# Optimization experiments

Hardware: AMD Instinct MI355X
Metric: run time of the kernel (lower is better)

The kernel has to match this reference:

```python
import jax, jax.numpy as jnp
import numpy as np

N = 50000        # nodes
E = 800000       # random edges (self loops appended inside reference, per PyG default)
IN = 128         # in_channels
H1, C1 = 8, 64   # conv1: heads, hidden_channels
NUM_CLASSES = 2  # conv2 out (heads=1, concat=False)
NEG_SLOPE = 0.2  # PyG GATConv default LeakyReLU slope


def setup_inputs() -> dict:
    key = jax.random.key(0)
    ks = jax.random.split(key, 12)
    x = jax.random.normal(ks[0], (N, IN), dtype=jnp.float32)
    edge_index = jax.random.randint(ks[1], (2, E), 0, N)
    # conv1 params: W1 [IN, H1*C1], att vectors [H1, C1], bias [H1*C1]
    W1 = jax.random.normal(ks[2], (IN, H1 * C1), dtype=jnp.float32) / np.sqrt(IN)
    a_src1 = jax.random.normal(ks[3], (H1, C1), dtype=jnp.float32) / np.sqrt(C1)
    a_dst1 = jax.random.normal(ks[4], (H1, C1), dtype=jnp.float32) / np.sqrt(C1)
    b1 = jnp.zeros((H1 * C1,), dtype=jnp.float32)
    # conv2 params: heads=1, out=NUM_CLASSES
    W2 = jax.random.normal(ks[5], (H1 * C1, 1 * NUM_CLASSES), dtype=jnp.float32) / np.sqrt(H1 * C1)
    a_src2 = jax.random.normal(ks[6], (1, NUM_CLASSES), dtype=jnp.float32) / np.sqrt(NUM_CLASSES)
    a_dst2 = jax.random.normal(ks[7], (1, NUM_CLASSES), dtype=jnp.float32) / np.sqrt(NUM_CLASSES)
    b2 = jnp.zeros((NUM_CLASSES,), dtype=jnp.float32)
    return {"x": x, "edge_index": edge_index, "W1": W1, "a_src1": a_src1,
            "a_dst1": a_dst1, "b1": b1, "W2": W2, "a_src2": a_src2,
            "a_dst2": a_dst2, "b2": b2}


def gat_layer(x, src, dst, W, a_src, a_dst, bias, concat):
    n = x.shape[0]
    heads, ch = a_src.shape
    h = (x @ W).reshape(n, heads, ch)                      # [N,H,C]
    alpha_s = jnp.einsum('nhc,hc->nh', h, a_src)           # per-node src score
    alpha_d = jnp.einsum('nhc,hc->nh', h, a_dst)           # per-node dst score
    e = jax.nn.leaky_relu(alpha_s[src] + alpha_d[dst], NEG_SLOPE)  # [Etot,H]
    # segment softmax over edges grouped by destination node
    m = jax.ops.segment_max(e, dst, num_segments=n)
    ex = jnp.exp(e - m[dst])
    den = jax.ops.segment_sum(ex, dst, num_segments=n)
    alpha = ex / den[dst]                                  # [Etot,H]
    out = jax.ops.segment_sum(h[src] * alpha[:, :, None], dst, num_segments=n)  # [N,H,C]
    out = out.reshape(n, heads * ch) if concat else out.mean(axis=1)
    return out + bias


def reference(x, edge_index, W1, a_src1, a_dst1, b1, W2, a_src2, a_dst2, b2):
    n = x.shape[0]
    loops = jnp.arange(n, dtype=edge_index.dtype)
    src = jnp.concatenate([edge_index[0], loops])   # PyG add_self_loops=True
    dst = jnp.concatenate([edge_index[1], loops])
    h = gat_layer(x, src, dst, W1, a_src1, a_dst1, b1, concat=True)   # [N, H1*C1]
    h = jax.nn.elu(h)
    # dropout is identity in eval mode
    out = gat_layer(h, src, dst, W2, a_src2, a_dst2, b2, concat=False)  # [N, 2]
    return out
```

## Files before the change

kernel.cpp:

```cpp
#include <hip/hip_runtime.h>
#include <hip/hip_bf16.h>

#define NEG 0.2f
#define BKT 64
#define DSTR 32

typedef __attribute__((ext_vector_type(8))) short bf16x8;
typedef __attribute__((ext_vector_type(4))) float f32x4;

static __device__ __forceinline__ unsigned short f2bf(float f) {
    union { float f; unsigned u; } v; v.f = f;
    unsigned r = v.u + 0x7fff + ((v.u >> 16) & 1);
    return (unsigned short)(r >> 16);
}
static __device__ __forceinline__ float bf_lo(unsigned u) {
    return __uint_as_float(u << 16);
}
static __device__ __forceinline__ float bf_hi(unsigned u) {
    return __uint_as_float(u & 0xffff0000u);
}

__global__ void k_init(int* __restrict__ deg, unsigned short* __restrict__ csr, int n) {
    int v = blockIdx.x * 256 + threadIdx.x;
    if (v >= n) return;
    deg[(size_t)v * DSTR] = 1;
    csr[(size_t)v * BKT] = (unsigned short)v;
}

__global__ __launch_bounds__(256) void k_big(const int* __restrict__ ei,
                                             int* __restrict__ deg,
                                             unsigned short* __restrict__ csr,
                                             const float* __restrict__ x,
                                             const float* __restrict__ W1,
                                             const float* __restrict__ a_src,
                                             const float* __restrict__ a_dst,
                                             unsigned short* __restrict__ h1b,
                                             float* __restrict__ as1,
                                             float* __restrict__ ad1,
                                             int E_, int n, int gblocks) {
    int tid = threadIdx.x;
    if ((int)blockIdx.x >= gblocks) {
        int e = (blockIdx.x - gblocks) * 256 + tid;
        if (e >= E_) return;
        int s = ei[e], d = ei[E_ + e];
        int slot = atomicAdd(&deg[(size_t)d * DSTR], 1);
        if (slot < BKT) csr[(size_t)d * BKT + slot] = (unsigned short)s;
        return;
    }
    __shared__ unsigned short stg[4][16][72];
    int wave = tid >> 6, lane = tid & 63;
    int l15 = lane & 15, q = lane >> 4;
    int rowblk = blockIdx.x * 256 + wave * 64;

    bf16x8 xf[4][4];
    #pragma unroll
    for (int st = 0; st < 4; st++) {
        int ar = rowblk + st * 16 + l15; if (ar > n - 1) ar = n - 1;
        const float* ap = x + (size_t)ar * 128 + q * 8;
        #pragma unroll
        for (int kb = 0; kb < 4; kb++) {
            float4 v0 = *(const float4*)(ap + kb * 32);
            float4 v1 = *(const float4*)(ap + kb * 32 + 4);
            xf[st][kb][0] = (short)f2bf(v0.x); xf[st][kb][1] = (short)f2bf(v0.y);
            xf[st][kb][2] = (short)f2bf(v0.z); xf[st][kb][3] = (short)f2bf(v0.w);
            xf[st][kb][4] = (short)f2bf(v1.x); xf[st][kb][5] = (short)f2bf(v1.y);
            xf[st][kb][6] = (short)f2bf(v1.z); xf[st][kb][7] = (short)f2bf(v1.w);
        }
    }

    for (int j = 0; j < 8; j++) {
        int col0 = j * 64;
        bf16x8 bfr[4][4];
        #pragma unroll
        for (int kb = 0; kb < 4; kb++)
            #pragma unroll
            for (int t = 0; t < 4; t++) {
                const float* wp = W1 + (size_t)(kb * 32 + q * 8) * 512 + col0 + t * 16 + l15;
                #pragma unroll
                for (int e = 0; e < 8; e++)
                    bfr[kb][t][e] = (short)f2bf(wp[(size_t)e * 512]);
            }
        float asv[4], adv[4];
        #pragma unroll
        for (int t = 0; t < 4; t++) {
            asv[t] = a_src[j * 64 + t * 16 + l15];
            adv[t] = a_dst[j * 64 + t * 16 + l15];
        }

        #pragma unroll
        for (int st = 0; st < 4; st++) {
            int row0 = rowblk + st * 16;
            f32x4 acc[4] = {};
            #pragma unroll
            for (int kb = 0; kb < 4; kb++)
                #pragma unroll
                for (int t = 0; t < 4; t++)
                    acc[t] = __builtin_amdgcn_mfma_f32_16x16x32_bf16(xf[st][kb], bfr[kb][t], acc[t], 0, 0, 0);
            #pragma unroll
            for (int t = 0; t < 4; t++)
                #pragma unroll
                for (int r = 0; r < 4; r++)
                    stg[wave][q * 4 + r][t * 16 + l15] = f2bf(acc[t][r]);
            #pragma unroll
            for (int p = 0; p < 2; p++) {
                int lr = p * 8 + (lane >> 3);
                int row = row0 + lr;
                int cd = (lane & 7) * 8;
                uint4 vv = *(const uint4*)&stg[wave][lr][cd];
                if (row < n)
                    *(uint4*)(h1b + (size_t)row * 512 + col0 + cd) = vv;
            }
            float ps[4], pd[4];
            #pragma unroll
            for (int r = 0; r < 4; r++) {
                ps[r] = acc[0][r] * asv[0] + acc[1][r] * asv[1]
                      + acc[2][r] * asv[2] + acc[3][r] * asv[3];
                pd[r] = acc[0][r] * adv[0] + acc[1][r] * adv[1]
                      + acc[2][r] * adv[2] + acc[3][r] * adv[3];
                #pragma unroll
                for (int off = 1; off < 16; off <<= 1) {
                    ps[r] += __shfl_xor(ps[r], off, 64);
                    pd[r] += __shfl_xor(pd[r], off, 64);
                }
            }
            if (l15 < 4) {
                int r = l15;
                float vps = ps[0], vpd = pd[0];
                if (r == 1) { vps = ps[1]; vpd = pd[1]; }
                if (r == 2) { vps = ps[2]; vpd = pd[2]; }
                if (r == 3) { vps = ps[3]; vpd = pd[3]; }
                int row = row0 + q * 4 + r;
                if (row < n) { as1[row * 8 + j] = vps; ad1[row * 8 + j] = vpd; }
            }
        }
    }
}

__global__ __launch_bounds__(256) void k_agg1(const unsigned short* __restrict__ h1b,
                                              const float* __restrict__ as1,
                                              const float* __restrict__ ad1,
                                              const float* __restrict__ b1,
                                              const float* __restrict__ W2,
                                              const int* __restrict__ deg,
                                              const unsigned short* __restrict__ csr,
                                              float* __restrict__ h2, int n) {
    int lane = threadIdx.x & 63;
    int v = blockIdx.x * 4 + (threadIdx.x >> 6);
    if (v >= n) return;
    int head = lane >> 3, c = lane * 8;
    int dv = deg[(size_t)v * DSTR]; if (dv > BKT) dv = BKT;
    const unsigned short* cp = csr + (size_t)v * BKT;
    float adh = ad1[v * 8 + head];
    float s = 0.f;
    float acc[8] = {};
    int i = 0;
    for (; i + 4 <= dv; i += 4) {
        ushort4 uu = *(const ushort4*)(cp + i);
        int u0 = uu.x, u1 = uu.y, u2 = uu.z, u3 = uu.w;
        float ea = as1[u0 * 8 + head] + adh;
        float eb = as1[u1 * 8 + head] + adh;
        float ec = as1[u2 * 8 + head] + adh;
        float ed = as1[u3 * 8 + head] + adh;
        uint4 h0 = *(const uint4*)(h1b + (size_t)u0 * 512 + c);
        uint4 h1 = *(const uint4*)(h1b + (size_t)u1 * 512 + c);
        uint4 h2v = *(const uint4*)(h1b + (size_t)u2 * 512 + c);
        uint4 h3 = *(const uint4*)(h1b + (size_t)u3 * 512 + c);
        ea = (ea >= 0.f) ? ea : NEG * ea;
        eb = (eb >= 0.f) ? eb : NEG * eb;
        ec = (ec >= 0.f) ? ec : NEG * ec;
        ed = (ed >= 0.f) ? ed : NEG * ed;
        float w0 = __expf(ea), w1 = __expf(eb), w2 = __expf(ec), w3 = __expf(ed);
        s += (w0 + w1) + (w2 + w3);
        acc[0] = fmaf(w3, bf_lo(h3.x), fmaf(w2, bf_lo(h2v.x), fmaf(w1, bf_lo(h1.x), fmaf(w0, bf_lo(h0.x), acc[0]))));
        acc[1] = fmaf(w3, bf_hi(h3.x), fmaf(w2, bf_hi(h2v.x), fmaf(w1, bf_hi(h1.x), fmaf(w0, bf_hi(h0.x), acc[1]))));
        acc[2] = fmaf(w3, bf_lo(h3.y), fmaf(w2, bf_lo(h2v.y), fmaf(w1, bf_lo(h1.y), fmaf(w0, bf_lo(h0.y), acc[2]))));
        acc[3] = fmaf(w3, bf_hi(h3.y), fmaf(w2, bf_hi(h2v.y), fmaf(w1, bf_hi(h1.y), fmaf(w0, bf_hi(h0.y), acc[3]))));
        acc[4] = fmaf(w3, bf_lo(h3.z), fmaf(w2, bf_lo(h2v.z), fmaf(w1, bf_lo(h1.z), fmaf(w0, bf_lo(h0.z), acc[4]))));
        acc[5] = fmaf(w3, bf_hi(h3.z), fmaf(w2, bf_hi(h2v.z), fmaf(w1, bf_hi(h1.z), fmaf(w0, bf_hi(h0.z), acc[5]))));
        acc[6] = fmaf(w3, bf_lo(h3.w), fmaf(w2, bf_lo(h2v.w), fmaf(w1, bf_lo(h1.w), fmaf(w0, bf_lo(h0.w), acc[6]))));
        acc[7] = fmaf(w3, bf_hi(h3.w), fmaf(w2, bf_hi(h2v.w), fmaf(w1, bf_hi(h1.w), fmaf(w0, bf_hi(h0.w), acc[7]))));
    }
    for (; i < dv; i++) {
        int u = cp[i];
        float e = as1[u * 8 + head] + adh;
        e = (e >= 0.f) ? e : NEG * e;
        float w = __expf(e);
        s += w;
        uint4 hv = *(const uint4*)(h1b + (size_t)u * 512 + c);
        acc[0] = fmaf(w, bf_lo(hv.x), acc[0]);
        acc[1] = fmaf(w, bf_hi(hv.x), acc[1]);
        acc[2] = fmaf(w, bf_lo(hv.y), acc[2]);
        acc[3] = fmaf(w, bf_hi(hv.y), acc[3]);
        acc[4] = fmaf(w, bf_lo(hv.z), acc[4]);
        acc[5] = fmaf(w, bf_hi(hv.z), acc[5]);
        acc[6] = fmaf(w, bf_lo(hv.w), acc[6]);
        acc[7] = fmaf(w, bf_hi(hv.w), acc[7]);
    }
    float inv = 1.0f / s;
    float4 ba = *(const float4*)(b1 + c);
    float4 bb = *(const float4*)(b1 + c + 4);
    float o[8] = {acc[0] * inv + ba.x, acc[1] * inv + ba.y,
                  acc[2] * inv + ba.z, acc[3] * inv + ba.w,
                  acc[4] * inv + bb.x, acc[5] * inv + bb.y,
                  acc[6] * inv + bb.z, acc[7] * inv + bb.w};
    #pragma unroll
    for (int jj = 0; jj < 8; jj++)
        o[jj] = (o[jj] > 0.f) ? o[jj] : (__expf(o[jj]) - 1.0f);
    const float4* wp = (const float4*)(W2 + c * 2);
    float4 w0 = wp[0], w1 = wp[1], w2 = wp[2], w3 = wp[3];
    float p0 = o[0] * w0.x + o[1] * w0.z + o[2] * w1.x + o[3] * w1.z
             + o[4] * w2.x + o[5] * w2.z + o[6] * w3.x + o[7] * w3.z;
    float p1 = o[0] * w0.y + o[1] * w0.w + o[2] * w1.y + o[3] * w1.w
             + o[4] * w2.y + o[5] * w2.w + o[6] * w3.y + o[7] * w3.w;
    #pragma unroll
    for (int off = 1; off < 64; off <<= 1) {
        p0 += __shfl_xor(p0, off, 64);
        p1 += __shfl_xor(p1, off, 64);
    }
    if (lane == 0) {
        h2[2 * v] = p0;
        h2[2 * v + 1] = p1;
    }
}

__global__ __launch_bounds__(256) void k_agg2(const float* __restrict__ h2,
                                              const float* __restrict__ a_src2,
                                              const float* __restrict__ a_dst2,
                                              const float* __restrict__ b2,
                                              const int* __restrict__ deg,
                                              const unsigned short* __restrict__ csr,
                                              float* __restrict__ out, int n) {
    int tid = threadIdx.x;
    int lane = tid & 63, wave = tid >> 6;
    int sub = lane & 7, g = lane >> 3;
    int v = blockIdx.x * 32 + wave * 8 + g;
    if (v >= n) return;
    int dv = deg[(size_t)v * DSTR]; if (dv > BKT) dv = BKT;
    const unsigned short* cp = csr + (size_t)v * BKT;
    float sa0 = a_src2[0], sa1 = a_src2[1];
    float da0 = a_dst2[0], da1 = a_dst2[1];
    float2 hv = *(const float2*)(h2 + 2 * v);
    float adv = hv.x * da0 + hv.y * da1;
    float s = 0.f, a0 = 0.f, a1 = 0.f;
    for (int i = sub; i < dv; i += 8) {
        int u = cp[i];
        float2 hu = *(const float2*)(h2 + 2 * u);
        float e = hu.x * sa0 + hu.y * sa1 + adv;
        e = (e >= 0.f) ? e : NEG * e;
        float w = __expf(e);
        s += w;
        a0 = fmaf(w, hu.x, a0);
        a1 = fmaf(w, hu.y, a1);
    }
    #pragma unroll
    for (int off = 1; off < 8; off <<= 1) {
        s  += __shfl_xor(s, off, 64);
        a0 += __shfl_xor(a0, off, 64);
        a1 += __shfl_xor(a1, off, 64);
    }
    if (sub == 0) {
        float inv = 1.0f / s;
        out[2 * v]     = a0 * inv + b2[0];
        out[2 * v + 1] = a1 * inv + b2[1];
    }
}

extern "C" void kernel_launch(void* const* d_in, const int* in_sizes, int n_in,
                              void* d_out, int out_size, void* d_ws, size_t ws_size,
                              hipStream_t stream) {
    const float* x      = (const float*)d_in[0];
    const int*   ei     = (const int*)d_in[1];
    const float* W1     = (const float*)d_in[2];
    const float* a_src1 = (const float*)d_in[3];
    const float* a_dst1 = (const float*)d_in[4];
    const float* b1     = (const float*)d_in[5];
    const float* W2     = (const float*)d_in[6];
    const float* a_src2 = (const float*)d_in[7];
    const float* a_dst2 = (const float*)d_in[8];
    const float* b2     = (const float*)d_in[9];
    float* out = (float*)d_out;

    int n  = in_sizes[0] / 128;
    int E_ = in_sizes[1] / 2;
    int rblk = (n + 255) / 256;
    int npad = rblk * 256;

    char* w = (char*)d_ws;
    auto alloc = [&](size_t bytes) {
        char* p = w; w += (bytes + 255) & ~(size_t)255; return p;
    };
    int*            deg    = (int*)alloc((size_t)n * DSTR * 4);
    unsigned short* csr    = (unsigned short*)alloc((size_t)n * BKT * 2);
    unsigned short* h1b    = (unsigned short*)alloc((size_t)npad * 512 * 2);
    float*          as1    = (float*)alloc((size_t)n * 8 * 4);
    float*          ad1    = (float*)alloc((size_t)n * 8 * 4);
    float*          h2     = (float*)alloc((size_t)n * 2 * 4);

    int nb256 = (n + 255) / 256;
    k_init<<<nb256, 256, 0, stream>>>(deg, csr, n);

    int gblocks = rblk;
    int sblocks = (E_ + 255) / 256;
    k_big<<<gblocks + sblocks, 256, 0, stream>>>(ei, deg, csr, x, W1,
                                                 a_src1, a_dst1, h1b, as1, ad1,
                                                 E_, n, gblocks);

    int nb = (n + 3) / 4;
    k_agg1<<<nb, 256, 0, stream>>>(h1b, as1, ad1, b1, W2, deg, csr, h2, n);

    int ab = (n + 31) / 32;
    k_agg2<<<ab, 256, 0, stream>>>(h2, a_src2, a_dst2, b2, deg, csr, out, n);
}
```

Before: 286.5 us.

## Pretranspose W1 to bf16 once and halve rows per GEMM block

k_init now also converts W1 to a transposed bf16 copy. The GEMM blocks can then load B fragments with one vector load each, instead of eight strided fp32 loads plus conversions per fragment. Each GEMM block now covers 128 rows instead of 256, which roughly doubles the number of blocks, and each scatter thread now handles two edges. The cost is that every GEMM block still reads all of W1, so total weight traffic rises with the block count, and k_init's fixed grid of 256 blocks assumes n is at most 65536.

```diff
diff --git a/kernel.cpp b/kernel.cpp
--- a/kernel.cpp
+++ b/kernel.cpp
@@ -20,18 +20,23 @@
     return __uint_as_float(u & 0xffff0000u);
 }
 
-__global__ void k_init(int* __restrict__ deg, unsigned short* __restrict__ csr, int n) {
+__global__ void k_init(int* __restrict__ deg, unsigned short* __restrict__ csr,
+                       const float* __restrict__ W1, unsigned short* __restrict__ W1bT,
+                       int n) {
     int v = blockIdx.x * 256 + threadIdx.x;
-    if (v >= n) return;
-    deg[(size_t)v * DSTR] = 1;
-    csr[(size_t)v * BKT] = (unsigned short)v;
+    if (v < n) {
+        deg[(size_t)v * DSTR] = 1;
+        csr[(size_t)v * BKT] = (unsigned short)v;
+    }
+    int col = v >> 7, row = v & 127;
+    W1bT[(size_t)col * 128 + row] = f2bf(W1[(size_t)row * 512 + col]);
 }
 
 __global__ __launch_bounds__(256) void k_big(const int* __restrict__ ei,
                                              int* __restrict__ deg,
                                              unsigned short* __restrict__ csr,
                                              const float* __restrict__ x,
-                                             const float* __restrict__ W1,
+                                             const unsigned short* __restrict__ W1bT,
                                              const float* __restrict__ a_src,
                                              const float* __restrict__ a_dst,
                                              unsigned short* __restrict__ h1b,
@@ -40,21 +45,28 @@
                                              int E_, int n, int gblocks) {
     int tid = threadIdx.x;
     if ((int)blockIdx.x >= gblocks) {
-        int e = (blockIdx.x - gblocks) * 256 + tid;
-        if (e >= E_) return;
-        int s = ei[e], d = ei[E_ + e];
-        int slot = atomicAdd(&deg[(size_t)d * DSTR], 1);
-        if (slot < BKT) csr[(size_t)d * BKT + slot] = (unsigned short)s;
+        int base = (blockIdx.x - gblocks) * 512 + tid;
+        if (base < E_) {
+            int s = ei[base], d = ei[E_ + base];
+            int slot = atomicAdd(&deg[(size_t)d * DSTR], 1);
+            if (slot < BKT) csr[(size_t)d * BKT + slot] = (unsigned short)s;
+        }
+        int e2 = base + 256;
+        if (e2 < E_) {
+            int s = ei[e2], d = ei[E_ + e2];
+            int slot = atomicAdd(&deg[(size_t)d * DSTR], 1);
+            if (slot < BKT) csr[(size_t)d * BKT + slot] = (unsigned short)s;
+        }
         return;
     }
     __shared__ unsigned short stg[4][16][72];
     int wave = tid >> 6, lane = tid & 63;
     int l15 = lane & 15, q = lane >> 4;
-    int rowblk = blockIdx.x * 256 + wave * 64;
-
-    bf16x8 xf[4][4];
+    int rowblk = blockIdx.x * 128 + wave * 32;
+
+    bf16x8 xf[2][4];
     #pragma unroll
-    for (int st = 0; st < 4; st++) {
+    for (int st = 0; st < 2; st++) {
         int ar = rowblk + st * 16 + l15; if (ar > n - 1) ar = n - 1;
         const float* ap = x + (size_t)ar * 128 + q * 8;
         #pragma unroll
@@ -74,12 +86,9 @@
         #pragma unroll
         for (int kb = 0; kb < 4; kb++)
             #pragma unroll
-            for (int t = 0; t < 4; t++) {
-                const float* wp = W1 + (size_t)(kb * 32 + q * 8) * 512 + col0 + t * 16 + l15;
-                #pragma unroll
-                for (int e = 0; e < 8; e++)
-                    bfr[kb][t][e] = (short)f2bf(wp[(size_t)e * 512]);
-            }
+            for (int t = 0; t < 4; t++)
+                bfr[kb][t] = *(const bf16x8*)(W1bT + (size_t)(col0 + t * 16 + l15) * 128
+                                              + kb * 32 + q * 8);
         float asv[4], adv[4];
         #pragma unroll
         for (int t = 0; t < 4; t++) {
@@ -88,7 +97,7 @@
         }
 
         #pragma unroll
-        for (int st = 0; st < 4; st++) {
+        for (int st = 0; st < 2; st++) {
             int row0 = rowblk + st * 16;
             f32x4 acc[4] = {};
             #pragma unroll
@@ -282,8 +291,8 @@
 
     int n  = in_sizes[0] / 128;
     int E_ = in_sizes[1] / 2;
-    int rblk = (n + 255) / 256;
-    int npad = rblk * 256;
+    int rblk = (n + 127) / 128;
+    int npad = rblk * 128;
 
     char* w = (char*)d_ws;
     auto alloc = [&](size_t bytes) {
@@ -292,16 +301,16 @@
     int*            deg    = (int*)alloc((size_t)n * DSTR * 4);
     unsigned short* csr    = (unsigned short*)alloc((size_t)n * BKT * 2);
     unsigned short* h1b    = (unsigned short*)alloc((size_t)npad * 512 * 2);
+    unsigned short* W1bT   = (unsigned short*)alloc((size_t)512 * 128 * 2);
     float*          as1    = (float*)alloc((size_t)n * 8 * 4);
     float*          ad1    = (float*)alloc((size_t)n * 8 * 4);
     float*          h2     = (float*)alloc((size_t)n * 2 * 4);
 
-    int nb256 = (n + 255) / 256;
-    k_init<<<nb256, 256, 0, stream>>>(deg, csr, n);
+    k_init<<<256, 256, 0, stream>>>(deg, csr, W1, W1bT, n);
 
     int gblocks = rblk;
-    int sblocks = (E_ + 255) / 256;
-    k_big<<<gblocks + sblocks, 256, 0, stream>>>(ei, deg, csr, x, W1,
+    int sblocks = (E_ + 511) / 512;
+    k_big<<<gblocks + sblocks, 256, 0, stream>>>(ei, deg, csr, x, W1bT,
                                                  a_src1, a_dst1, h1b, as1, ad1,
                                                  E_, n, gblocks);
 
```

Result: no change. 283.9 us, median of 2 (-0.9%).
